# Kernel tuning notes

Measured on AMD Instinct MI355X. Metric: run time of the kernel, lower is better.

Reference implementation:

```python
import jax, jax.numpy as jnp
import numpy as np

B, T0, H0, W0 = 16, 8, 14, 14
DIM = 768
HEADS = 8
HD = DIM // HEADS  # 96
N = T0 * H0 * W0 + 1  # 1569 (cls token)
STRIDE_Q = (1, 1, 1)
STRIDE_KV = (1, 2, 2)
REL_SP_DIM = 2 * max(H0, H0 // 2) - 1  # 27
REL_T_DIM = 2 * T0 - 1  # 15
LN_EPS = 1e-5


def _rel_idx(q, k):
    # decomposed relative-position index table (static, numpy)
    q_ratio = max(k / q, 1.0)
    k_ratio = max(q / k, 1.0)
    d = np.arange(q)[:, None] * q_ratio - np.arange(k)[None, :] * k_ratio
    d += (k - 1) * k_ratio
    return d.astype(np.int64)


def _layernorm(x, g, b):
    m = jnp.mean(x, axis=-1, keepdims=True)
    v = jnp.mean((x - m) ** 2, axis=-1, keepdims=True)
    return (x - m) * jax.lax.rsqrt(v + LN_EPS) * g + b


def _attention_pool(t, w, thw, stride, g, b):
    # t: [B, heads, 1+L, C]; depthwise 3x3x3 conv over THW, cls token bypasses pool
    cls_tok, body = t[:, :, :1], t[:, :, 1:]
    Bb, NH, L, C = body.shape
    T, H, W = thw
    x = body.reshape(Bb * NH, T, H, W, C).transpose(0, 4, 1, 2, 3)  # NCDHW
    y = jax.lax.conv_general_dilated(
        x, w, window_strides=stride, padding=[(1, 1), (1, 1), (1, 1)],
        feature_group_count=C, dimension_numbers=('NCDHW', 'OIDHW', 'NCDHW'))
    nT, nH, nW = y.shape[2], y.shape[3], y.shape[4]
    y = y.reshape(Bb, NH, C, nT * nH * nW).transpose(0, 1, 3, 2)
    y = jnp.concatenate([cls_tok, y], axis=2)
    return _layernorm(y, g, b), (nT, nH, nW)


def setup_inputs() -> dict:
    key = jax.random.key(0)
    ks = jax.random.split(key, 12)
    s = 0.02
    inp = {
        'x': jax.random.normal(ks[0], (B, N, DIM), jnp.float32),
        'qkv_w': jax.random.normal(ks[1], (DIM, 3 * DIM), jnp.float32) * s,
        'qkv_b': jax.random.normal(ks[2], (3 * DIM,), jnp.float32) * s,
        'pool_q_w': jax.random.normal(ks[3], (HD, 1, 3, 3, 3), jnp.float32) * s,
        'pool_k_w': jax.random.normal(ks[4], (HD, 1, 3, 3, 3), jnp.float32) * s,
        'pool_v_w': jax.random.normal(ks[5], (HD, 1, 3, 3, 3), jnp.float32) * s,
        'ln_q_g': jnp.ones((HD,), jnp.float32), 'ln_q_b': jnp.zeros((HD,), jnp.float32),
        'ln_k_g': jnp.ones((HD,), jnp.float32), 'ln_k_b': jnp.zeros((HD,), jnp.float32),
        'ln_v_g': jnp.ones((HD,), jnp.float32), 'ln_v_b': jnp.zeros((HD,), jnp.float32),
        'rel_pos_h': jax.random.normal(ks[6], (REL_SP_DIM, HD), jnp.float32) * s,
        'rel_pos_w': jax.random.normal(ks[7], (REL_SP_DIM, HD), jnp.float32) * s,
        'rel_pos_t': jax.random.normal(ks[8], (REL_T_DIM, HD), jnp.float32) * s,
        'proj_w': jax.random.normal(ks[9], (DIM, DIM), jnp.float32) * s,
        'proj_b': jax.random.normal(ks[10], (DIM,), jnp.float32) * s,
        'thw_t': T0, 'thw_h': H0, 'thw_w': W0,
    }
    return inp


def reference(x, qkv_w, qkv_b, pool_q_w, pool_k_w, pool_v_w,
              ln_q_g, ln_q_b, ln_k_g, ln_k_b, ln_v_g, ln_v_b,
              rel_pos_h, rel_pos_w, rel_pos_t, proj_w, proj_b,
              thw_t, thw_h, thw_w):
    thw = (int(thw_t), int(thw_h), int(thw_w))
    Bb, Nn, _ = x.shape
    qkv = (x @ qkv_w + qkv_b).reshape(Bb, Nn, 3, HEADS, HD).transpose(2, 0, 3, 1, 4)
    q, k, v = qkv[0], qkv[1], qkv[2]  # [B, H, N, hd]
    q, q_shape = _attention_pool(q, pool_q_w, thw, STRIDE_Q, ln_q_g, ln_q_b)
    k, k_shape = _attention_pool(k, pool_k_w, thw, STRIDE_KV, ln_k_g, ln_k_b)
    v, _ = _attention_pool(v, pool_v_w, thw, STRIDE_KV, ln_v_g, ln_v_b)
    qt, qh, qw = q_shape
    kt, kh, kw = k_shape
    scale = HD ** -0.5
    attn = jnp.einsum('bhqc,bhkc->bhqk', q * scale, k)  # [B,H,1+Lq,1+Lk]
    # spatial + temporal decomposed relative position bias (cls row/col excluded)
    Rh = rel_pos_h[_rel_idx(qh, kh)]  # [qh,kh,hd]
    Rw = rel_pos_w[_rel_idx(qw, kw)]  # [qw,kw,hd]
    Rt = rel_pos_t[_rel_idx(qt, kt)]  # [qt,kt,hd]
    r_q = q[:, :, 1:].reshape(Bb, HEADS, qt, qh, qw, HD)
    rel_h = jnp.einsum('bythwc,hkc->bythwk', r_q, Rh)  # [B,H,qt,qh,qw,kh]
    rel_w = jnp.einsum('bythwc,wkc->bythwk', r_q, Rw)  # [B,H,qt,qh,qw,kw]
    rel_t = jnp.einsum('bnthwc,tkc->bnthwk', r_q, Rt)  # [B,H,qt,qh,qw,kt]
    bias = (rel_h[:, :, :, :, :, None, :, None]
            + rel_w[:, :, :, :, :, None, None, :]
            + rel_t[:, :, :, :, :, :, None, None])  # [B,H,qt,qh,qw,kt,kh,kw]
    attn = attn.at[:, :, 1:, 1:].add(bias.reshape(Bb, HEADS, qt * qh * qw, kt * kh * kw))
    attn = jax.nn.softmax(attn, axis=-1)
    out = jnp.einsum('bhqk,bhkc->bhqc', attn, v)
    out = out.at[:, :, 1:].add(q[:, :, 1:])  # residual pooling (skip cls)
    out = out.transpose(0, 2, 1, 3).reshape(Bb, -1, DIM)
    out = out @ proj_w + proj_b
    return out
```

## Files before the change

### kernel.cpp

```cpp
#include <hip/hip_runtime.h>
#include <hip/hip_bf16.h>

typedef __hip_bfloat16 bf16;
typedef __attribute__((ext_vector_type(8))) short bf16x8;
typedef __attribute__((ext_vector_type(4))) float f32x4;

#define B_     16
#define N_     1569
#define DIM_   768
#define NHEADS 8
#define HD_    96
#define LK_    393
#define T0_    8
#define H0_    14
#define W0_    14

struct __align__(8) bf16x4s { bf16 a, b, c, d; };

__device__ __forceinline__ float b2f(unsigned short u) {
  union { unsigned int i; float f; } x;
  x.i = ((unsigned int)u) << 16;
  return x.f;
}

__global__ __launch_bounds__(256) void cvt_f32_bf16(
    const float* __restrict__ in, bf16* __restrict__ out, int n4) {
  int i = blockIdx.x * 256 + threadIdx.x;
  if (i < n4) {
    float4 v = ((const float4*)in)[i];
    bf16x4s o{__float2bfloat16(v.x), __float2bfloat16(v.y),
              __float2bfloat16(v.z), __float2bfloat16(v.w)};
    ((bf16x4s*)out)[i] = o;
  }
}

__global__ __launch_bounds__(256) void transpose_f32_bf16(
    const float* __restrict__ in, bf16* __restrict__ out, int R, int C) {
  __shared__ float tile[32][33];
  int c0 = blockIdx.x * 32, r0 = blockIdx.y * 32;
  int tx = threadIdx.x, ty = threadIdx.y;
  for (int i = 0; i < 32; i += 8) {
    int r = r0 + ty + i, c = c0 + tx;
    if (r < R && c < C) tile[ty + i][tx] = in[(size_t)r * C + c];
  }
  __syncthreads();
  for (int i = 0; i < 32; i += 8) {
    int c = c0 + ty + i, r = r0 + tx;
    if (c < C && r < R) out[(size_t)c * R + r] = __float2bfloat16(tile[tx][ty + i]);
  }
}

__global__ __launch_bounds__(256) void prep_pw(
    const float* __restrict__ wq, const float* __restrict__ wk,
    const float* __restrict__ wv, float* __restrict__ outp) {
  int i = blockIdx.x * 256 + threadIdx.x;
  if (i < 2592) {
    int widx = i / 96, x = i % 96;
    outp[i]        = wq[x * 27 + widx];
    outp[2592 + i] = wk[x * 27 + widx];
    outp[5184 + i] = wv[x * 27 + widx];
  }
}

__device__ __forceinline__ void gl_lds16(const bf16* g, bf16* l) {
  __builtin_amdgcn_global_load_lds(
      (const __attribute__((address_space(1))) void*)g,
      (__attribute__((address_space(3))) void*)l, 16, 0, 0);
}

template <typename OutT>
__global__ __launch_bounds__(256) void gemm_bt(
    const bf16* __restrict__ A, const bf16* __restrict__ BT,
    const float* __restrict__ bias, OutT* __restrict__ C,
    int M, int Nn, int K) {
  constexpr int BM = 128, BN = 128, BK = 32;
  __shared__ __align__(16) bf16 As[BM][BK];
  __shared__ __align__(16) bf16 Bs[BN][BK];
  const int tid = threadIdx.x;
  const int lane = tid & 63, wave = tid >> 6;
  const int bm = blockIdx.x * BM, bn = blockIdx.y * BN;
  const int wm = (wave >> 1) * 64, wn = (wave & 1) * 64;
  const int lrow = lane >> 2;
  const int lcol = (lane & 3) * 8;

  f32x4 acc[4][4];
#pragma unroll
  for (int i = 0; i < 4; ++i)
#pragma unroll
    for (int j = 0; j < 4; ++j) acc[i][j] = (f32x4){0.f, 0.f, 0.f, 0.f};

  for (int k0 = 0; k0 < K; k0 += BK) {
#pragma unroll
    for (int r = 0; r < 2; ++r) {
      int arow = bm + wave * 32 + r * 16 + lrow;
      if (arow >= M) arow = M - 1;
      gl_lds16(A + (size_t)arow * K + k0 + lcol, &As[wave * 32 + r * 16][0]);
      int brow = bn + wave * 32 + r * 16 + lrow;
      gl_lds16(BT + (size_t)brow * K + k0 + lcol, &Bs[wave * 32 + r * 16][0]);
    }
    __syncthreads();
    const int fr = lane & 15, kg = (lane >> 4) * 8;
    bf16x8 af[4], bfr[4];
#pragma unroll
    for (int i = 0; i < 4; ++i) {
      af[i] = *(const bf16x8*)&As[wm + i * 16 + fr][kg];
      bfr[i] = *(const bf16x8*)&Bs[wn + i * 16 + fr][kg];
    }
#pragma unroll
    for (int i = 0; i < 4; ++i)
#pragma unroll
      for (int j = 0; j < 4; ++j)
        acc[i][j] = __builtin_amdgcn_mfma_f32_16x16x32_bf16(af[i], bfr[j],
                                                            acc[i][j], 0, 0, 0);
    __syncthreads();
  }

  const int fr = lane & 15, rg = (lane >> 4) * 4;
#pragma unroll
  for (int j = 0; j < 4; ++j) {
    int col = bn + wn + j * 16 + fr;
    float bv = bias[col];
#pragma unroll
    for (int i = 0; i < 4; ++i) {
#pragma unroll
      for (int r = 0; r < 4; ++r) {
        int row = bm + wm + i * 16 + rg + r;
        if (row < M)
          C[(size_t)row * Nn + col] = (OutT)(acc[i][j][r] + bv);
      }
    }
  }
}

__global__ __launch_bounds__(256) void pool_ln(
    const bf16* __restrict__ qkv, const float* __restrict__ pwT,
    const float* __restrict__ g, const float* __restrict__ bt,
    bf16* __restrict__ outp, int which, int sHW, int oH, int oW, int Lout) {
  __shared__ float pwl[27 * 104];
  const int tid = threadIdx.x;
  for (int i = tid; i < 2592; i += 256) {
    int widx = i / 96, c = i % 96;
    int cgi = c >> 3, j = c & 7;
    pwl[widx * 104 + cgi * 8 + (cgi >> 2) * 4 + j] = pwT[i];
  }
  __syncthreads();

  const int rloc = tid >> 4;
  const int cg = tid & 15;
  const int orow = blockIdx.x * 16 + rloc;
  if (orow >= Lout) return;
  const int bh = blockIdx.y;
  const int b = bh >> 3, h = bh & 7;
  const bool act = (cg < 12);
  const bf16* base =
      qkv + (size_t)b * N_ * 2304 + which * 768 + h * 96 + cg * 8;

  float acc[8];
#pragma unroll
  for (int j = 0; j < 8; ++j) acc[j] = 0.f;

  if (act) {
    if (orow == 0) {
      union { uint4 u; bf16 e[8]; } tv;
      tv.u = *(const uint4*)base;
#pragma unroll
      for (int j = 0; j < 8; ++j) acc[j] = (float)tv.e[j];
    } else {
      int pos = orow - 1;
      int ot = pos / (oH * oW), r = pos % (oH * oW);
      int oh = r / oW, ow = r % oW;
      const float* wrow = pwl + cg * 8 + (cg >> 2) * 4;
#pragma unroll
      for (int kt = 0; kt < 3; ++kt) {
        int it = ot + kt - 1;
        if (it < 0 || it >= T0_) continue;
#pragma unroll
        for (int kh = 0; kh < 3; ++kh) {
          int ih = oh * sHW + kh - 1;
          if (ih < 0 || ih >= H0_) continue;
#pragma unroll
          for (int kw = 0; kw < 3; ++kw) {
            int iw = ow * sHW + kw - 1;
            if (iw < 0 || iw >= W0_) continue;
            int n = 1 + (it * H0_ + ih) * W0_ + iw;
            int widx = (kt * 3 + kh) * 3 + kw;
            union { uint4 u; bf16 e[8]; } tv;
            tv.u = *(const uint4*)(base + (size_t)n * 2304);
            const float* w = wrow + widx * 104;
            float wv_[8];
            *(float4*)&wv_[0] = *(const float4*)w;
            *(float4*)&wv_[4] = *(const float4*)(w + 4);
#pragma unroll
            for (int j = 0; j < 8; ++j) acc[j] += (float)tv.e[j] * wv_[j];
          }
        }
      }
    }
  }

  float s = 0.f, s2 = 0.f;
#pragma unroll
  for (int j = 0; j < 8; ++j) { s += acc[j]; s2 += acc[j] * acc[j]; }
#pragma unroll
  for (int mk = 1; mk < 16; mk <<= 1) {
    s += __shfl_xor(s, mk);
    s2 += __shfl_xor(s2, mk);
  }
  float mean = s * (1.f / 96.f);
  float var = s2 * (1.f / 96.f) - mean * mean;
  float rstd = rsqrtf(var + 1e-5f);

  if (act) {
    float gv[8], bv[8];
    *(float4*)&gv[0] = *(const float4*)(g + cg * 8);
    *(float4*)&gv[4] = *(const float4*)(g + cg * 8 + 4);
    *(float4*)&bv[0] = *(const float4*)(bt + cg * 8);
    *(float4*)&bv[4] = *(const float4*)(bt + cg * 8 + 4);
    union { uint4 u; bf16 e[8]; } ov;
#pragma unroll
    for (int j = 0; j < 8; ++j)
      ov.e[j] = __float2bfloat16((acc[j] - mean) * rstd * gv[j] + bv[j]);
    *(uint4*)(outp + ((size_t)bh * Lout + orow) * 96 + cg * 8) = ov.u;
  }
}

__global__ __launch_bounds__(256) void rel_dots(
    const bf16* __restrict__ qp, const float* __restrict__ rpt,
    const float* __restrict__ rph, const float* __restrict__ rpw,
    float* __restrict__ relq) {
  __shared__ float tab[69 * 100];
  __shared__ __align__(16) bf16 Qls[64][96];
  const int tid = threadIdx.x;
  const int bh = blockIdx.y;
  const int q0 = blockIdx.x * 64;
  const bf16* qb = qp + (size_t)bh * N_ * HD_;

  for (int i = tid; i < 69 * 24; i += 256) {
    int row = i / 24, c4 = (i % 24) * 4;
    const float* src = row < 15 ? rpt + row * 96
                      : row < 42 ? rph + (row - 15) * 96
                                 : rpw + (row - 42) * 96;
    *(float4*)&tab[row * 100 + c4] = *(const float4*)(src + c4);
  }
  for (int c = tid; c < 768; c += 256) {
    int row = c / 12, seg = c % 12;
    int p = q0 + row;
    if (p >= N_) p = N_ - 1;
    *(uint4*)&Qls[row][seg * 8] = *(const uint4*)(qb + (size_t)p * HD_ + seg * 8);
  }
  __syncthreads();

  const int r8 = tid >> 5, slot = tid & 31;
  if (slot == 15 || slot >= 23) return;
  for (int g = 0; g < 8; ++g) {
    int row = g * 8 + r8;
    int p = q0 + row;
    if (p < 1 || p >= N_) continue;
    int pos = p - 1;
    int qt = pos / 196, rr = pos % 196;
    int qh = rr / 14, qw = rr % 14;
    int ti = slot < 8 ? qt - slot + 7
            : slot < 15 ? 15 + (qh - 2 * (slot - 8) + 12)
                        : 42 + (qw - 2 * (slot - 16) + 12);
    const float* trow = &tab[ti * 100];
    float acc = 0.f;
#pragma unroll
    for (int d4 = 0; d4 < 24; ++d4) {
      float4 w = *(const float4*)(trow + d4 * 4);
      union { uint2 u; unsigned short s[4]; } qv;
      qv.u = *(const uint2*)&Qls[row][d4 * 4];
      acc += w.x * b2f(qv.s[0]) + w.y * b2f(qv.s[1]) +
             w.z * b2f(qv.s[2]) + w.w * b2f(qv.s[3]);
    }
    relq[((size_t)bh * N_ + p) * 24 + slot] = acc;
  }
}

__global__ __launch_bounds__(256) void attn_fused(
    const bf16* __restrict__ qp, const bf16* __restrict__ kp,
    const bf16* __restrict__ vp, const float* __restrict__ relq,
    bf16* __restrict__ aout) {
  __shared__ __align__(16) bf16 Ks[64][104];
  __shared__ __align__(16) bf16 VtS[96 * 64];
  __shared__ __align__(16) bf16 Ps[4][16][72];
  __shared__ float relb[64][24];

  const int tid = threadIdx.x;
  const int wv = tid >> 6, lane = tid & 63;
  const int col = lane & 15, quad = lane >> 4;
  const int bh = blockIdx.y;
  const int b = bh >> 3;
  const int h = bh & 7;
  const int q0 = blockIdx.x * 64;
  const bf16* qb = qp + (size_t)bh * N_ * HD_;
  const bf16* kb = kp + (size_t)bh * LK_ * HD_;
  const bf16* vb = vp + (size_t)bh * LK_ * HD_;
  const float scale = 0.102062072615966f;

  {
    int nrow = N_ - q0;
    if (nrow > 64) nrow = 64;
    int n4 = nrow * 6;
    const uint4* src = (const uint4*)(relq + ((size_t)bh * N_ + q0) * 24);
    for (int i = tid; i < n4; i += 256) ((uint4*)relb)[i] = src[i];
  }

  int qrow = q0 + wv * 16 + col;
  if (qrow >= N_) qrow = N_ - 1;
  bf16x8 qa[3];
#pragma unroll
  for (int ks_ = 0; ks_ < 3; ++ks_)
    qa[ks_] = *(const bf16x8*)(qb + (size_t)qrow * HD_ + ks_ * 32 + quad * 8);

  float mrun[4] = {-1e30f, -1e30f, -1e30f, -1e30f};
  float lrun[4] = {0.f, 0.f, 0.f, 0.f};
  f32x4 oacc[6];
#pragma unroll
  for (int dt = 0; dt < 6; ++dt) oacc[dt] = (f32x4){0.f, 0.f, 0.f, 0.f};

  for (int kt_i = 0; kt_i < 7; ++kt_i) {
    const int kt0 = kt_i * 64;
    __syncthreads();
    for (int c = tid; c < 768; c += 256) {
      int row = c / 12, seg = c % 12;
      int key = kt0 + row;
      if (key >= LK_) key = LK_ - 1;
      *(uint4*)&Ks[row][seg * 8] =
          *(const uint4*)(kb + (size_t)key * HD_ + seg * 8);
      union { uint4 u; bf16 e[8]; } tv;
      tv.u = *(const uint4*)(vb + (size_t)key * HD_ + seg * 8);
#pragma unroll
      for (int j = 0; j < 8; ++j) {
        int d = seg * 8 + j;
        int c_ = (d ^ (d >> 3)) & 7;
        VtS[d * 64 + (row ^ (c_ << 3))] = tv.e[j];
      }
    }
    __syncthreads();

    f32x4 sacc[4];
#pragma unroll
    for (int jt = 0; jt < 4; ++jt) sacc[jt] = (f32x4){0.f, 0.f, 0.f, 0.f};
#pragma unroll
    for (int ks_ = 0; ks_ < 3; ++ks_) {
#pragma unroll
      for (int jt = 0; jt < 4; ++jt) {
        bf16x8 bk = *(const bf16x8*)&Ks[jt * 16 + col][ks_ * 32 + quad * 8];
        sacc[jt] = __builtin_amdgcn_mfma_f32_16x16x32_bf16(qa[ks_], bk, sacc[jt], 0, 0, 0);
      }
    }

    float sv[4][4];
#pragma unroll
    for (int jt = 0; jt < 4; ++jt) {
      int kglob = kt0 + jt * 16 + col;
      bool kvalid = (kglob < LK_);
      int kbod = (kglob >= 1) ? kglob - 1 : 0;
      int kt_ = kbod / 49, krem = kbod % 49;
      int kh_ = krem / 7, kw_ = krem % 7;
#pragma unroll
      for (int r = 0; r < 4; ++r) {
        int qr = wv * 16 + quad * 4 + r;
        int p = q0 + qr;
        float s = sacc[jt][r] * scale;
        if (kvalid && kglob >= 1 && p >= 1 && p < N_)
          s += relb[qr][kt_] + relb[qr][8 + kh_] + relb[qr][16 + kw_];
        if (!kvalid) s = -1e30f;
        sv[jt][r] = s;
      }
    }

    float pexp[4][4];
#pragma unroll
    for (int r = 0; r < 4; ++r) {
      float pm = fmaxf(fmaxf(sv[0][r], sv[1][r]), fmaxf(sv[2][r], sv[3][r]));
#pragma unroll
      for (int mk = 1; mk < 16; mk <<= 1) pm = fmaxf(pm, __shfl_xor(pm, mk));
      float mn = fmaxf(mrun[r], pm);
      float alpha = __expf(mrun[r] - mn);
      mrun[r] = mn;
      float rs = 0.f;
#pragma unroll
      for (int jt = 0; jt < 4; ++jt) {
        float e = __expf(sv[jt][r] - mn);
        pexp[jt][r] = e;
        rs += e;
      }
#pragma unroll
      for (int mk = 1; mk < 16; mk <<= 1) rs += __shfl_xor(rs, mk);
      lrun[r] = lrun[r] * alpha + rs;
#pragma unroll
      for (int dt = 0; dt < 6; ++dt) {
        oacc[dt][r] *= alpha;
      }
    }

#pragma unroll
    for (int jt = 0; jt < 4; ++jt)
#pragma unroll
      for (int r = 0; r < 4; ++r)
        Ps[wv][quad * 4 + r][jt * 16 + col] = __float2bfloat16(pexp[jt][r]);

#pragma unroll
    for (int ks_ = 0; ks_ < 2; ++ks_) {
      bf16x8 ap = *(const bf16x8*)&Ps[wv][col][ks_ * 32 + quad * 8];
#pragma unroll
      for (int dt = 0; dt < 6; ++dt) {
        int d = dt * 16 + col;
        int c_ = (d ^ (d >> 3)) & 7;
        bf16x8 bv =
            *(const bf16x8*)&VtS[d * 64 + ((ks_ * 32 + quad * 8) ^ (c_ << 3))];
        oacc[dt] = __builtin_amdgcn_mfma_f32_16x16x32_bf16(ap, bv, oacc[dt], 0, 0, 0);
      }
    }
  }

#pragma unroll
  for (int r = 0; r < 4; ++r) {
    int qr = wv * 16 + quad * 4 + r;
    int p = q0 + qr;
    if (p >= N_) continue;
    float inv = 1.f / lrun[r];
#pragma unroll
    for (int dt = 0; dt < 6; ++dt) {
      int d = dt * 16 + col;
      float val = oacc[dt][r] * inv;
      if (p >= 1) val += (float)qb[(size_t)p * HD_ + d];
      aout[((size_t)b * N_ + p) * DIM_ + h * HD_ + d] = __float2bfloat16(val);
    }
  }
}

extern "C" void kernel_launch(void* const* d_in, const int* in_sizes, int n_in,
                              void* d_out, int out_size, void* d_ws,
                              size_t ws_size, hipStream_t stream) {
  (void)in_sizes; (void)n_in; (void)out_size; (void)ws_size;
  const float* x      = (const float*)d_in[0];
  const float* qkv_w  = (const float*)d_in[1];
  const float* qkv_b  = (const float*)d_in[2];
  const float* pool_q = (const float*)d_in[3];
  const float* pool_k = (const float*)d_in[4];
  const float* pool_v = (const float*)d_in[5];
  const float* ln_q_g = (const float*)d_in[6];
  const float* ln_q_b = (const float*)d_in[7];
  const float* ln_k_g = (const float*)d_in[8];
  const float* ln_k_b = (const float*)d_in[9];
  const float* ln_v_g = (const float*)d_in[10];
  const float* ln_v_b = (const float*)d_in[11];
  const float* rph    = (const float*)d_in[12];
  const float* rpw    = (const float*)d_in[13];
  const float* rpt    = (const float*)d_in[14];
  const float* proj_w = (const float*)d_in[15];
  const float* proj_b = (const float*)d_in[16];

  char* ws = (char*)d_ws;
  bf16* wt_qkv  = (bf16*)(ws);
  bf16* wt_proj = (bf16*)(ws + 3538944);
  bf16* xb      = (bf16*)(ws + 4718592);
  bf16* aout    = xb;
  bf16* qkv     = (bf16*)(ws + 43278336);
  float* relq   = (float*)(ws + 43278336);
  bf16* qpoolb  = (bf16*)(ws + 158957568);
  bf16* kpoolb  = (bf16*)(ws + 197517312);
  bf16* vpoolb  = (bf16*)(ws + 207175680);
  float* pwT    = (float*)(ws + 216834048);
  float* outp   = (float*)d_out;

  int n4 = (B_ * N_ * DIM_) / 4;
  cvt_f32_bf16<<<(n4 + 255) / 256, 256, 0, stream>>>(x, xb, n4);
  transpose_f32_bf16<<<dim3(72, 24), dim3(32, 8), 0, stream>>>(qkv_w, wt_qkv, 768, 2304);
  transpose_f32_bf16<<<dim3(24, 24), dim3(32, 8), 0, stream>>>(proj_w, wt_proj, 768, 768);
  prep_pw<<<11, 256, 0, stream>>>(pool_q, pool_k, pool_v, pwT);

  gemm_bt<bf16><<<dim3(197, 18), 256, 0, stream>>>(xb, wt_qkv, qkv_b, qkv,
                                                   B_ * N_, 3 * DIM_, DIM_);

  pool_ln<<<dim3(99, 128), 256, 0, stream>>>(qkv, pwT, ln_q_g, ln_q_b, qpoolb,
                                             0, 1, 14, 14, N_);
  pool_ln<<<dim3(25, 128), 256, 0, stream>>>(qkv, pwT + 2592, ln_k_g, ln_k_b,
                                             kpoolb, 1, 2, 7, 7, LK_);
  pool_ln<<<dim3(25, 128), 256, 0, stream>>>(qkv, pwT + 5184, ln_v_g, ln_v_b,
                                             vpoolb, 2, 2, 7, 7, LK_);

  rel_dots<<<dim3(25, 128), 256, 0, stream>>>(qpoolb, rpt, rph, rpw, relq);

  attn_fused<<<dim3(25, 128), 256, 0, stream>>>(qpoolb, kpoolb, vpoolb, relq,
                                                aout);

  gemm_bt<float><<<dim3(197, 6), 256, 0, stream>>>(aout, wt_proj, proj_b, outp,
                                                   B_ * N_, DIM_, DIM_);
}
```

Baseline: 827.6 us.

## Deepen GEMM K tile, swizzle LDS layout, remap blocks per XCD

The bf16 GEMM now stages a K depth of 64 per iteration instead of 32. This halves the number of barrier pairs per K loop. The LDS tiles use an XOR swizzle on the 16-byte column chunk so that MFMA fragment reads avoid bank conflicts. The grid is flattened to 1D, and block ids are remapped so that consecutive tiles land on the same XCD for better L2 reuse. In exchange, LDS use per block doubles, which may reduce occupancy.

```diff
diff --git a/kernel.cpp b/kernel.cpp
--- a/kernel.cpp
+++ b/kernel.cpp
@@ -73,15 +73,22 @@
     const bf16* __restrict__ A, const bf16* __restrict__ BT,
     const float* __restrict__ bias, OutT* __restrict__ C,
     int M, int Nn, int K) {
-  constexpr int BM = 128, BN = 128, BK = 32;
+  constexpr int BM = 128, BN = 128, BK = 64;
   __shared__ __align__(16) bf16 As[BM][BK];
   __shared__ __align__(16) bf16 Bs[BN][BK];
   const int tid = threadIdx.x;
   const int lane = tid & 63, wave = tid >> 6;
-  const int bm = blockIdx.x * BM, bn = blockIdx.y * BN;
+
+  const int nNp = Nn >> 7;
+  const int nwg = gridDim.x;
+  const int q8 = nwg >> 3, r8 = nwg & 7;
+  const int xcd = blockIdx.x & 7, idx = blockIdx.x >> 3;
+  const int w = (xcd < r8 ? xcd * (q8 + 1) : r8 * (q8 + 1) + (xcd - r8) * q8) + idx;
+  const int bm = (w / nNp) * BM, bn = (w % nNp) * BN;
+
   const int wm = (wave >> 1) * 64, wn = (wave & 1) * 64;
-  const int lrow = lane >> 2;
-  const int lcol = (lane & 3) * 8;
+  const int sl = lane >> 3;
+  const int sc = ((lane & 7) ^ sl) * 8;
 
   f32x4 acc[4][4];
 #pragma unroll
@@ -91,27 +98,32 @@
 
   for (int k0 = 0; k0 < K; k0 += BK) {
 #pragma unroll
-    for (int r = 0; r < 2; ++r) {
-      int arow = bm + wave * 32 + r * 16 + lrow;
+    for (int c = 0; c < 4; ++c) {
+      int r0 = wave * 32 + c * 8;
+      int arow = bm + r0 + sl;
       if (arow >= M) arow = M - 1;
-      gl_lds16(A + (size_t)arow * K + k0 + lcol, &As[wave * 32 + r * 16][0]);
-      int brow = bn + wave * 32 + r * 16 + lrow;
-      gl_lds16(BT + (size_t)brow * K + k0 + lcol, &Bs[wave * 32 + r * 16][0]);
+      gl_lds16(A + (size_t)arow * K + k0 + sc, &As[r0][0]);
+      int brow = bn + r0 + sl;
+      gl_lds16(BT + (size_t)brow * K + k0 + sc, &Bs[r0][0]);
     }
     __syncthreads();
-    const int fr = lane & 15, kg = (lane >> 4) * 8;
-    bf16x8 af[4], bfr[4];
-#pragma unroll
-    for (int i = 0; i < 4; ++i) {
-      af[i] = *(const bf16x8*)&As[wm + i * 16 + fr][kg];
-      bfr[i] = *(const bf16x8*)&Bs[wn + i * 16 + fr][kg];
-    }
-#pragma unroll
-    for (int i = 0; i < 4; ++i)
-#pragma unroll
-      for (int j = 0; j < 4; ++j)
-        acc[i][j] = __builtin_amdgcn_mfma_f32_16x16x32_bf16(af[i], bfr[j],
-                                                            acc[i][j], 0, 0, 0);
+    const int fr = lane & 15, q = lane >> 4;
+#pragma unroll
+    for (int ks = 0; ks < 2; ++ks) {
+      const int ph = (((ks << 2) + q) ^ (fr & 7)) << 3;
+      bf16x8 af[4], bfr[4];
+#pragma unroll
+      for (int i = 0; i < 4; ++i) {
+        af[i] = *(const bf16x8*)&As[wm + i * 16 + fr][ph];
+        bfr[i] = *(const bf16x8*)&Bs[wn + i * 16 + fr][ph];
+      }
+#pragma unroll
+      for (int i = 0; i < 4; ++i)
+#pragma unroll
+        for (int j = 0; j < 4; ++j)
+          acc[i][j] = __builtin_amdgcn_mfma_f32_16x16x32_bf16(af[i], bfr[j],
+                                                              acc[i][j], 0, 0, 0);
+    }
     __syncthreads();
   }
 
@@ -472,8 +484,8 @@
   transpose_f32_bf16<<<dim3(24, 24), dim3(32, 8), 0, stream>>>(proj_w, wt_proj, 768, 768);
   prep_pw<<<11, 256, 0, stream>>>(pool_q, pool_k, pool_v, pwT);
 
-  gemm_bt<bf16><<<dim3(197, 18), 256, 0, stream>>>(xb, wt_qkv, qkv_b, qkv,
-                                                   B_ * N_, 3 * DIM_, DIM_);
+  gemm_bt<bf16><<<197 * 18, 256, 0, stream>>>(xb, wt_qkv, qkv_b, qkv,
+                                              B_ * N_, 3 * DIM_, DIM_);
 
   pool_ln<<<dim3(99, 128), 256, 0, stream>>>(qkv, pwT, ln_q_g, ln_q_b, qpoolb,
                                              0, 1, 14, 14, N_);
@@ -487,6 +499,6 @@
   attn_fused<<<dim3(25, 128), 256, 0, stream>>>(qpoolb, kpoolb, vpoolb, relq,
                                                 aout);
 
-  gemm_bt<float><<<dim3(197, 6), 256, 0, stream>>>(aout, wt_proj, proj_b, outp,
-                                                   B_ * N_, DIM_, DIM_);
-}
+  gemm_bt<float><<<197 * 6, 256, 0, stream>>>(aout, wt_proj, proj_b, outp,
+                                              B_ * N_, DIM_, DIM_);
+}
```

Measured after the change: 794.2 us. -4.0%, faster.
